# Kernel optimization log

Hardware: AMD Instinct MI355X
Metric: run time of the kernel (lower is better)

The kernel has to match this reference:

```python
import jax, jax.numpy as jnp
import numpy as np

EPS = 1e-6          # numerical floor for norms / denominators (fp32-safe)
PROJ_EPS = 1e-5     # ball projection margin: max norm = 1 - PROJ_EPS


def _norm(x):
    return jnp.sqrt(jnp.maximum(jnp.sum(x * x, axis=-1, keepdims=True), EPS * EPS))


def hyp_proj(x):
    # project onto open Poincare ball of radius 1 - PROJ_EPS
    n = _norm(x)
    scale = jnp.minimum((1.0 - PROJ_EPS) / n, 1.0)
    return x * scale


def exp_map_zero(v):
    n = _norm(v)
    return jnp.tanh(n) * v / n


def log_map_zero(y):
    n = _norm(y)
    return jnp.arctanh(jnp.minimum(n, 1.0 - PROJ_EPS)) * y / n


def mobius_add(x, y):
    x2 = jnp.sum(x * x, axis=-1, keepdims=True)
    y2 = jnp.sum(y * y, axis=-1, keepdims=True)
    xy = jnp.sum(x * y, axis=-1, keepdims=True)
    num = (1.0 + 2.0 * xy + y2) * x + (1.0 - x2) * y
    den = 1.0 + 2.0 * xy + x2 * y2
    return num / jnp.maximum(den, EPS)


def gcn_layer(x, rows, cols, vals, W, b, n_nodes, use_act):
    # tangent-space linear transform
    pre = log_map_zero(x)                      # [N, d]
    h = pre @ W                                # [N, d]
    # sparse adjacency matmul: agg[r] += val * h[c]
    msg = vals[:, None] * h[cols]              # [E, d]
    agg = jax.ops.segment_sum(msg, rows, num_segments=n_nodes)
    out = hyp_proj(exp_map_zero(agg))
    # hyperbolic bias via mobius addition
    bh = hyp_proj(exp_map_zero(b[None, :]))    # [1, d]
    out = hyp_proj(mobius_add(out, bh))
    if use_act:
        out = hyp_proj(exp_map_zero(jnp.tanh(log_map_zero(out))))
    return out


def setup_inputs() -> dict:
    key = jax.random.key(0)
    N, D, E = 100000, 64, 3200000
    ks = jax.random.split(key, 8)
    x = jax.random.normal(ks[0], (N, D), dtype=jnp.float32) * 0.1
    edge_vals = jax.random.uniform(ks[1], (E,), dtype=jnp.float32)
    W1 = jax.random.normal(ks[2], (D, D), dtype=jnp.float32) * (1.0 / np.sqrt(D))
    b1 = jnp.zeros((D,), dtype=jnp.float32)
    W2 = jax.random.normal(ks[3], (D, D), dtype=jnp.float32) * (1.0 / np.sqrt(D))
    b2 = jnp.zeros((D,), dtype=jnp.float32)
    edge_rows = jax.random.randint(ks[4], (E,), 0, N, dtype=jnp.int64 if jax.config.jax_enable_x64 else jnp.int32).astype(jnp.int32)
    edge_cols = jax.random.randint(ks[5], (E,), 0, N, dtype=jnp.int32)
    return {"x": x, "edge_vals": edge_vals, "W1": W1, "b1": b1,
            "W2": W2, "b2": b2, "edge_rows": edge_rows, "edge_cols": edge_cols}


def reference(x, edge_vals, W1, b1, W2, b2, edge_rows, edge_cols):
    n_nodes = x.shape[0]
    # HyperKA._graph_convolution: project base embeddings, then layers with
    # mobius residual; last layer has no activation.
    e0 = hyp_proj(x)
    h1 = gcn_layer(e0, edge_rows, edge_cols, edge_vals, W1, b1, n_nodes, use_act=True)
    h1 = hyp_proj(mobius_add(h1, e0))
    h2 = gcn_layer(h1, edge_rows, edge_cols, edge_vals, W2, b2, n_nodes, use_act=False)
    h2 = hyp_proj(mobius_add(h2, h1))
    return h2
```

## Files before the change

### kernel.cpp

```cpp
#include <hip/hip_runtime.h>
#include <math.h>

#define D 64
#define EPSF 1e-6f
#define EPS2F 1e-12f
#define PROJ_EPSF 1e-5f
#define EPB 16384

typedef _Float16 f16;
typedef f16 f16x4 __attribute__((ext_vector_type(4)));
typedef f16 f16x8 __attribute__((ext_vector_type(8)));
typedef float f32x4 __attribute__((ext_vector_type(4)));

__device__ __forceinline__ float frcp(float x)  { return __builtin_amdgcn_rcpf(x); }
__device__ __forceinline__ float fsqrt(float x) { return __builtin_amdgcn_sqrtf(x); }
__device__ __forceinline__ float ftanh(float x) {
    float e = __expf(2.0f * x);
    return (e - 1.0f) * frcp(e + 1.0f);
}
__device__ __forceinline__ float fatanh(float z) {
    return 0.5f * __logf((1.0f + z) * frcp(1.0f - z));
}

__device__ __forceinline__ float wave_sum(float v) {
#pragma unroll
    for (int o = 32; o > 0; o >>= 1) v += __shfl_xor(v, o, 64);
    return v;
}
__device__ __forceinline__ float qsum(float v) {
#pragma unroll
    for (int o = 1; o < 16; o <<= 1) v += __shfl_xor(v, o, 64);
    return v;
}

__global__ __launch_bounds__(256) void k1_hist_pre(
    const int* __restrict__ rows, const float* __restrict__ x,
    const float* __restrict__ b1, const float* __restrict__ b2,
    int* __restrict__ histT, f16* __restrict__ pre,
    float* __restrict__ nbuf, float* __restrict__ bhbuf,
    int E, int N, int nb1, int NBIN)
{
    const int bid = blockIdx.x, tid = threadIdx.x;
    const int lane = tid & 63;
    if (bid < nb1) {
        __shared__ int lh[512];
        for (int i = tid; i < NBIN; i += 256) lh[i] = 0;
        __syncthreads();
        const int e0 = bid * EPB;
#pragma unroll 4
        for (int k = 0; k < EPB / 256; ++k) {
            int e = e0 + k * 256 + tid;
            if (e < E) atomicAdd(&lh[__builtin_nontemporal_load(rows + e) >> 8], 1);
        }
        __syncthreads();
        for (int i = tid; i < NBIN; i += 256) histT[i * nb1 + bid] = lh[i];
    } else if (bid == nb1) {
        if (tid < 128) {
            int wsel = tid >> 6;
            const float* b = wsel ? b2 : b1;
            float bv = b[lane];
            float nb = fsqrt(fmaxf(wave_sum(bv * bv), EPS2F));
            float t = ftanh(nb);
            float v = bv * (t * frcp(nb));
            float nv = t;
            float sc = fminf((1.0f - PROJ_EPSF) * frcp(fmaxf(nv, EPSF)), 1.0f);
            v *= sc; nv = fminf(nv, 1.0f - PROJ_EPSF);
            bhbuf[wsel * 64 + lane] = v;
            if (lane == 0) bhbuf[128 + wsel] = nv;
        }
    } else {
        int node = (bid - nb1 - 1) * 4 + (tid >> 6);
        if (node >= N) return;
        float xv = x[(size_t)node * D + lane];
        float nx = fsqrt(fmaxf(wave_sum(xv * xv), EPS2F));
        float sc = fminf((1.0f - PROJ_EPSF) * frcp(nx), 1.0f);
        float e0 = xv * sc;
        float ne0 = fminf(nx, 1.0f - PROJ_EPSF);
        pre[(size_t)node * D + lane] = (f16)(e0 * (fatanh(ne0) * frcp(fmaxf(ne0, EPSF))));
        if (lane == 0) nbuf[node] = nx;
    }
}

__global__ __launch_bounds__(64) void scan_parts(int* __restrict__ part, int P)
{
    int lane = threadIdx.x;
    int carry = 0;
    for (int b = 0; b < P; b += 64) {
        int i = b + lane;
        int v = (i < P) ? part[i] : 0;
        int inc = v;
#pragma unroll
        for (int off = 1; off < 64; off <<= 1) {
            int tu = __shfl_up(inc, off, 64);
            if (lane >= off) inc += tu;
        }
        if (i < P) part[i] = inc - v + carry;
        carry += __shfl(inc, 63, 64);
    }
}

__global__ __launch_bounds__(256) void scan_apply(
    int* __restrict__ a, const int* __restrict__ part, int L)
{
    __shared__ int wbase[4];
    int t = threadIdx.x, lane = t & 63, wid = t >> 6;
    int idx0 = blockIdx.x * 1024 + t * 4;
    int v0 = 0, v1 = 0, v2 = 0, v3 = 0;
    if (idx0 < L) { int4 v = *(const int4*)(a + idx0); v0 = v.x; v1 = v.y; v2 = v.z; v3 = v.w; }
    int s = v0 + v1 + v2 + v3;
    int inc = s;
#pragma unroll
    for (int off = 1; off < 64; off <<= 1) {
        int tu = __shfl_up(inc, off, 64);
        if (lane >= off) inc += tu;
    }
    if (lane == 63) wbase[wid] = inc;
    __syncthreads();
    if (t == 0) { int acc = 0; for (int k = 0; k < 4; ++k) { int xx = wbase[k]; wbase[k] = acc; acc += xx; } }
    __syncthreads();
    int excl = part[blockIdx.x] + wbase[wid] + (inc - s);
    if (idx0 < L) {
        int4 o; o.x = excl; o.y = excl + v0; o.z = excl + v0 + v1; o.w = excl + v0 + v1 + v2;
        *(int4*)(a + idx0) = o;
    }
}

__device__ __forceinline__ void gemm64_body(
    const f16* __restrict__ A, const float* __restrict__ W,
    f16* __restrict__ C, int M, int wid, int nwaves, int lane)
{
    const int m = lane & 15;
    const int quad = lane >> 4;
    f16x8 Bfr[2][4];
#pragma unroll
    for (int kt = 0; kt < 2; ++kt)
#pragma unroll
        for (int nt = 0; nt < 4; ++nt) {
            f16x8 tmp;
#pragma unroll
            for (int j = 0; j < 8; ++j)
                tmp[j] = (f16)W[(kt * 32 + quad * 8 + j) * D + nt * 16 + m];
            Bfr[kt][nt] = tmp;
        }
    const int ntile = M >> 4;
    for (int tile = wid; tile < ntile; tile += nwaves) {
        const f16* arow = A + (size_t)(tile * 16 + m) * D;
        f16x8 a0 = *(const f16x8*)(arow + quad * 8);
        f16x8 a1 = *(const f16x8*)(arow + 32 + quad * 8);
#pragma unroll
        for (int nt = 0; nt < 4; ++nt) {
            f32x4 z = {0.0f, 0.0f, 0.0f, 0.0f};
            z = __builtin_amdgcn_mfma_f32_16x16x32_f16(a0, Bfr[0][nt], z, 0, 0, 0);
            z = __builtin_amdgcn_mfma_f32_16x16x32_f16(a1, Bfr[1][nt], z, 0, 0, 0);
#pragma unroll
            for (int r = 0; r < 4; ++r)
                C[(size_t)(tile * 16 + quad * 4 + r) * D + nt * 16 + m] = (f16)z[r];
        }
    }
}

__global__ __launch_bounds__(256) void k2_reduce_gemm(
    const int* __restrict__ histT, int* __restrict__ part, int Lp, int P,
    const f16* __restrict__ A, const float* __restrict__ W,
    f16* __restrict__ C, int M)
{
    const int tid = threadIdx.x, lane = tid & 63, wid4 = tid >> 6;
    if ((int)blockIdx.x < P) {
        __shared__ int ws[4];
        int idx0 = blockIdx.x * 1024 + tid * 4;
        int s = 0;
        if (idx0 < Lp) { int4 v = *(const int4*)(histT + idx0); s = v.x + v.y + v.z + v.w; }
        s = (int)wave_sum((float)s);
        if (lane == 0) ws[wid4] = s;
        __syncthreads();
        if (tid == 0) part[blockIdx.x] = ws[0] + ws[1] + ws[2] + ws[3];
    } else {
        int wid = (blockIdx.x - P) * 4 + wid4;
        int nwaves = (gridDim.x - P) * 4;
        gemm64_body(A, W, C, M, wid, nwaves, lane);
    }
}

__global__ __launch_bounds__(256) void gemm64(
    const f16* __restrict__ A, const float* __restrict__ W,
    f16* __restrict__ C, int M)
{
    gemm64_body(A, W, C, M, blockIdx.x * 4 + (threadIdx.x >> 6), gridDim.x * 4,
                threadIdx.x & 63);
}

__global__ __launch_bounds__(512) void p1_scatter(
    const int* __restrict__ rows, const int* __restrict__ cols,
    const float* __restrict__ vals, const int* __restrict__ histT,
    unsigned int* __restrict__ pay, unsigned char* __restrict__ rloc,
    int E, int nb1, int NBIN)
{
    __shared__ unsigned int  stage[512][32];
    __shared__ unsigned char srloc[512][32];
    __shared__ int gbase[512];
    __shared__ int cnt[512];
    __shared__ int flushed[512];
    __shared__ unsigned int msk[512];

    const int bid = blockIdx.x, tid = threadIdx.x;
    {
        int i = tid;
        gbase[i] = (i < NBIN) ? histT[i * nb1 + bid] : 0;
        cnt[i] = 0; flushed[i] = 0; msk[i] = 0u;
    }
    __syncthreads();

    const int e0 = bid * EPB;
    for (int rnd = 0; rnd < EPB / 2048; ++rnd) {
        int rr[4], cc[4]; float vv[4];
#pragma unroll
        for (int u = 0; u < 4; ++u) {
            int e = e0 + rnd * 2048 + u * 512 + tid;
            bool ok = e < E;
            rr[u] = ok ? __builtin_nontemporal_load(rows + e) : -1;
            cc[u] = ok ? __builtin_nontemporal_load(cols + e) : 0;
            vv[u] = ok ? __builtin_nontemporal_load(vals + e) : 0.0f;
        }
#pragma unroll
        for (int u = 0; u < 4; ++u) {
            if (rr[u] < 0) continue;
            int bin = rr[u] >> 8;
            unsigned int q = (unsigned int)fmaf(vv[u], 32767.0f, 0.5f);
            unsigned int p = (q << 17) | (unsigned int)cc[u];
            unsigned char rl = (unsigned char)(rr[u] & 255);
            int slot = atomicAdd(&cnt[bin], 1);
            if (slot - flushed[bin] < 32) {
                stage[bin][slot & 31] = p;
                srloc[bin][slot & 31] = rl;
                atomicOr(&msk[bin], 1u << (slot & 31));
            } else {
                int gp = gbase[bin] + slot;
                pay[gp] = p;
                rloc[gp] = rl;
            }
        }
        __syncthreads();
        if (tid < NBIN) {
            const int b = tid;
            int f = flushed[b];
            int n = cnt[b];
            unsigned int m = msk[b];
            const int gb = gbase[b];
            while (n - f >= 16) {
                const int half = (f >> 4) & 1;
                const unsigned int m16 = (m >> (half * 16)) & 0xFFFFu;
                const int base = gb + f;
                const int r0 = half * 16;
                if (m16 == 0xFFFFu) {
#pragma unroll
                    for (int k2 = 0; k2 < 16; ++k2)
                        pay[base + k2] = stage[b][r0 + k2];
#pragma unroll
                    for (int k2 = 0; k2 < 16; ++k2)
                        rloc[base + k2] = srloc[b][r0 + k2];
                } else {
                    for (int k2 = 0; k2 < 16; ++k2)
                        if (m16 & (1u << k2)) {
                            pay[base + k2] = stage[b][r0 + k2];
                            rloc[base + k2] = srloc[b][r0 + k2];
                        }
                }
                m &= ~(0xFFFFu << (half * 16));
                f += 16;
            }
            flushed[b] = f;
            msk[b] = m;
        }
        __syncthreads();
    }
    if (tid < NBIN) {
        const int b = tid;
        int f = flushed[b];
        const int n = cnt[b];
        const unsigned int m = msk[b];
        const int gb = gbase[b];
        for (; f < n; ++f) {
            if (m & (1u << (f & 31))) {
                pay[gb + f] = stage[b][f & 31];
                rloc[gb + f] = srloc[b][f & 31];
            }
        }
    }
}

__global__ __launch_bounds__(256) void band_build(
    const unsigned int* __restrict__ pay, const unsigned char* __restrict__ rloc,
    const int* __restrict__ histT, int* __restrict__ rs,
    unsigned int* __restrict__ epack, int E, int nb1, int NBIN, int N)
{
    __shared__ int lh[256];
    __shared__ int cur[256];
    __shared__ int wsum[4];
    const int b = blockIdx.x, tid = threadIdx.x;
    const int lane = tid & 63, wid = tid >> 6;
    const int segstart = histT[b * nb1];
    const int segend = (b + 1 < NBIN) ? histT[(b + 1) * nb1] : E;
    lh[tid] = 0;
    __syncthreads();
    for (int j = segstart + tid; j < segend; j += 256)
        atomicAdd(&lh[rloc[j]], 1);
    __syncthreads();
    int v = lh[tid];
    int inc = v;
#pragma unroll
    for (int off = 1; off < 64; off <<= 1) {
        int tu = __shfl_up(inc, off, 64);
        if (lane >= off) inc += tu;
    }
    if (lane == 63) wsum[wid] = inc;
    __syncthreads();
    int base = 0;
    for (int w2 = 0; w2 < wid; ++w2) base += wsum[w2];
    int excl = base + inc - v;
    cur[tid] = excl;
    int r = b * 256 + tid;
    if (r < N) rs[r] = segstart + excl + v;
    __syncthreads();
    for (int j = segstart + tid; j < segend; j += 256) {
        int pos = segstart + atomicAdd(&cur[rloc[j]], 1);
        epack[pos] = pay[j];
    }
}

__device__ __forceinline__ void csr_accum4(
    const int* __restrict__ rs, const unsigned int* __restrict__ epack,
    const f16* __restrict__ h, int row, int li, int qbase, float* a)
{
    const int start = (row == 0) ? 0 : rs[row - 1];
    const int end = rs[row];
    int nbat = (end - start + 15) >> 4;
#pragma unroll
    for (int o = 16; o < 64; o <<= 1) {
        int nbo = __shfl_xor(nbat, o, 64);
        nbat = nbo > nbat ? nbo : nbat;
    }
    const f16x4* __restrict__ h4 = (const f16x4*)h;
    float A0[4] = {0.f, 0.f, 0.f, 0.f}, A1[4] = {0.f, 0.f, 0.f, 0.f};
    for (int bb = 0; bb < nbat; ++bb) {
        int j = start + bb * 16 + li;
        unsigned int p = (j < end) ? epack[j] : 0u;
        int c = (int)(p & 131071u);
        float vf = (float)(p >> 17) * (1.0f / 32767.0f);
#pragma unroll
        for (int t = 0; t < 16; t += 2) {
            int   c0 = __shfl(c, qbase + t, 64);
            float v0 = __shfl(vf, qbase + t, 64);
            int   c1 = __shfl(c, qbase + t + 1, 64);
            float v1 = __shfl(vf, qbase + t + 1, 64);
            f16x4 h0 = h4[(size_t)c0 * 16 + li];
            f16x4 h1 = h4[(size_t)c1 * 16 + li];
#pragma unroll
            for (int k = 0; k < 4; ++k) {
                A0[k] = fmaf(v0, (float)h0[k], A0[k]);
                A1[k] = fmaf(v1, (float)h1[k], A1[k]);
            }
        }
    }
#pragma unroll
    for (int k = 0; k < 4; ++k) a[k] = A0[k] + A1[k];
}

__global__ __launch_bounds__(256) void layer1_fused(
    const int* __restrict__ rs, const unsigned int* __restrict__ epack,
    const f16* __restrict__ h, const float* __restrict__ x,
    const float* __restrict__ bhbuf, float* __restrict__ nbuf,
    f16* __restrict__ h1_out, f16* __restrict__ pre2_out, int N)
{
    const int lane = threadIdx.x & 63;
    const int q = lane >> 4, li = lane & 15, qbase = q << 4;
    int row = blockIdx.x * 16 + (threadIdx.x >> 6) * 4 + q;
    if (row >= N) row = N - 1;

    float a[4];
    csr_accum4(rs, epack, h, row, li, qbase, a);

    float na = fsqrt(fmaxf(qsum(a[0]*a[0] + a[1]*a[1] + a[2]*a[2] + a[3]*a[3]), EPS2F));
    float t = ftanh(na);
    float s = t * frcp(na);
    float o[4];
#pragma unroll
    for (int k = 0; k < 4; ++k) o[k] = a[k] * s;
    float no = t;
    float sc = fminf((1.0f - PROJ_EPSF) * frcp(fmaxf(no, EPSF)), 1.0f);
#pragma unroll
    for (int k = 0; k < 4; ++k) o[k] *= sc;
    no = fminf(no, 1.0f - PROJ_EPSF);

    float4 bp4 = ((const float4*)bhbuf)[li];
    float bh[4] = {bp4.x, bp4.y, bp4.z, bp4.w};
    float nbh = bhbuf[128];
    float xy = qsum(o[0]*bh[0] + o[1]*bh[1] + o[2]*bh[2] + o[3]*bh[3]);
    float x2 = no * no, y2 = nbh * nbh;
    float rd = frcp(fmaxf(1.0f + 2.0f * xy + x2 * y2, EPSF));
    float al = (1.0f + 2.0f * xy + y2) * rd;
    float be = (1.0f - x2) * rd;
    float m[4];
#pragma unroll
    for (int k = 0; k < 4; ++k) m[k] = al * o[k] + be * bh[k];
    float nm = fsqrt(fmaxf(al*al*x2 + be*be*y2 + 2.0f*al*be*xy, EPS2F));
    sc = fminf((1.0f - PROJ_EPSF) * frcp(fmaxf(nm, EPSF)), 1.0f);
#pragma unroll
    for (int k = 0; k < 4; ++k) m[k] *= sc;
    nm = fminf(nm, 1.0f - PROJ_EPSF);

    float lg = fatanh(nm) * frcp(fmaxf(nm, EPSF));
    float w[4];
#pragma unroll
    for (int k = 0; k < 4; ++k) w[k] = ftanh(m[k] * lg);
    float nw = fsqrt(fmaxf(qsum(w[0]*w[0] + w[1]*w[1] + w[2]*w[2] + w[3]*w[3]), EPS2F));
    float tw = ftanh(nw);
    s = tw * frcp(nw);
    float ov[4];
#pragma unroll
    for (int k = 0; k < 4; ++k) ov[k] = w[k] * s;
    float nov = tw;
    sc = fminf((1.0f - PROJ_EPSF) * frcp(fmaxf(nov, EPSF)), 1.0f);
#pragma unroll
    for (int k = 0; k < 4; ++k) ov[k] *= sc;
    nov = fminf(nov, 1.0f - PROJ_EPSF);

    float4 xp4 = ((const float4*)(x + (size_t)row * D))[li];
    float xp[4] = {xp4.x, xp4.y, xp4.z, xp4.w};
    float nx = nbuf[row];
    float sce = fminf((1.0f - PROJ_EPSF) * frcp(nx), 1.0f);
    float e0[4];
#pragma unroll
    for (int k = 0; k < 4; ++k) e0[k] = xp[k] * sce;
    float ne0 = fminf(nx, 1.0f - PROJ_EPSF);
    float xy2 = qsum(ov[0]*e0[0] + ov[1]*e0[1] + ov[2]*e0[2] + ov[3]*e0[3]);
    x2 = nov * nov; y2 = ne0 * ne0;
    rd = frcp(fmaxf(1.0f + 2.0f * xy2 + x2 * y2, EPSF));
    al = (1.0f + 2.0f * xy2 + y2) * rd;
    be = (1.0f - x2) * rd;
    float h1v[4];
#pragma unroll
    for (int k = 0; k < 4; ++k) h1v[k] = al * ov[k] + be * e0[k];
    float nh = fsqrt(fmaxf(al*al*x2 + be*be*y2 + 2.0f*al*be*xy2, EPS2F));
    sc = fminf((1.0f - PROJ_EPSF) * frcp(fmaxf(nh, EPSF)), 1.0f);
#pragma unroll
    for (int k = 0; k < 4; ++k) h1v[k] *= sc;
    nh = fminf(nh, 1.0f - PROJ_EPSF);

    f16x4 hp, pp;
    float lg2 = fatanh(nh) * frcp(fmaxf(nh, EPSF));
#pragma unroll
    for (int k = 0; k < 4; ++k) { hp[k] = (f16)h1v[k]; pp[k] = (f16)(h1v[k] * lg2); }
    ((f16x4*)h1_out)[(size_t)row * 16 + li] = hp;
    ((f16x4*)pre2_out)[(size_t)row * 16 + li] = pp;
    if (li == 0) nbuf[row] = nh;
}

__global__ __launch_bounds__(256) void layer2_fused(
    const int* __restrict__ rs, const unsigned int* __restrict__ epack,
    const f16* __restrict__ h2lin, const float* __restrict__ bhbuf,
    const float* __restrict__ nbuf, f16* __restrict__ h1_inout, int N)
{
    const int lane = threadIdx.x & 63;
    const int q = lane >> 4, li = lane & 15, qbase = q << 4;
    int row = blockIdx.x * 16 + (threadIdx.x >> 6) * 4 + q;
    if (row >= N) row = N - 1;

    float a[4];
    csr_accum4(rs, epack, h2lin, row, li, qbase, a);

    float na = fsqrt(fmaxf(qsum(a[0]*a[0] + a[1]*a[1] + a[2]*a[2] + a[3]*a[3]), EPS2F));
    float t = ftanh(na);
    float s = t * frcp(na);
    float o[4];
#pragma unroll
    for (int k = 0; k < 4; ++k) o[k] = a[k] * s;
    float no = t;
    float sc = fminf((1.0f - PROJ_EPSF) * frcp(fmaxf(no, EPSF)), 1.0f);
#pragma unroll
    for (int k = 0; k < 4; ++k) o[k] *= sc;
    no = fminf(no, 1.0f - PROJ_EPSF);

    float4 bp4 = ((const float4*)(bhbuf + 64))[li];
    float bh[4] = {bp4.x, bp4.y, bp4.z, bp4.w};
    float nbh = bhbuf[129];
    float xy = qsum(o[0]*bh[0] + o[1]*bh[1] + o[2]*bh[2] + o[3]*bh[3]);
    float x2 = no * no, y2 = nbh * nbh;
    float rd = frcp(fmaxf(1.0f + 2.0f * xy + x2 * y2, EPSF));
    float al = (1.0f + 2.0f * xy + y2) * rd;
    float be = (1.0f - x2) * rd;
    float m[4];
#pragma unroll
    for (int k = 0; k < 4; ++k) m[k] = al * o[k] + be * bh[k];
    float nm = fsqrt(fmaxf(al*al*x2 + be*be*y2 + 2.0f*al*be*xy, EPS2F));
    sc = fminf((1.0f - PROJ_EPSF) * frcp(fmaxf(nm, EPSF)), 1.0f);
#pragma unroll
    for (int k = 0; k < 4; ++k) m[k] *= sc;
    nm = fminf(nm, 1.0f - PROJ_EPSF);

    f16x4 hp = ((const f16x4*)h1_inout)[(size_t)row * 16 + li];
    float h1v[4] = {(float)hp[0], (float)hp[1], (float)hp[2], (float)hp[3]};
    float nh = nbuf[row];
    float xy2 = qsum(m[0]*h1v[0] + m[1]*h1v[1] + m[2]*h1v[2] + m[3]*h1v[3]);
    x2 = nm * nm; y2 = nh * nh;
    rd = frcp(fmaxf(1.0f + 2.0f * xy2 + x2 * y2, EPSF));
    al = (1.0f + 2.0f * xy2 + y2) * rd;
    be = (1.0f - x2) * rd;
    float r[4];
#pragma unroll
    for (int k = 0; k < 4; ++k) r[k] = al * m[k] + be * h1v[k];
    float n2 = fsqrt(fmaxf(al*al*x2 + be*be*y2 + 2.0f*al*be*xy2, EPS2F));
    sc = fminf((1.0f - PROJ_EPSF) * frcp(fmaxf(n2, EPSF)), 1.0f);
    f16x4 op;
#pragma unroll
    for (int k = 0; k < 4; ++k) op[k] = (f16)(r[k] * sc);
    ((f16x4*)h1_inout)[(size_t)row * 16 + li] = op;
}

__global__ __launch_bounds__(256) void expand4(
    const f16* __restrict__ src, float* __restrict__ dst, int n4)
{
    int i = blockIdx.x * 256 + threadIdx.x;
    if (i < n4) {
        f16x4 v = ((const f16x4*)src)[i];
        float4 o; o.x = (float)v[0]; o.y = (float)v[1]; o.z = (float)v[2]; o.w = (float)v[3];
        ((float4*)dst)[i] = o;
    }
}

extern "C" void kernel_launch(void* const* d_in, const int* in_sizes, int n_in,
                              void* d_out, int out_size, void* d_ws, size_t ws_size,
                              hipStream_t stream) {
    const float* x    = (const float*)d_in[0];
    const float* vals = (const float*)d_in[1];
    const float* W1   = (const float*)d_in[2];
    const float* b1   = (const float*)d_in[3];
    const float* W2   = (const float*)d_in[4];
    const float* b2   = (const float*)d_in[5];
    const int* rows   = (const int*)d_in[6];
    const int* cols   = (const int*)d_in[7];
    float* out = (float*)d_out;

    const int N = in_sizes[0] / D;
    const int E = in_sizes[1];
    const size_t nd = (size_t)N * D;

    const int NBIN = (N + 255) >> 8;
    const int nb1  = (E + EPB - 1) / EPB;
    const int L    = NBIN * nb1;
    const int Lp   = ((L + 1023) / 1024) * 1024;
    const int P    = Lp / 1024;

    char* w = (char*)d_ws;
    unsigned int*  epack = (unsigned int*)w;
    unsigned int*  pay   = (unsigned int*)(w + (size_t)E * 4);
    f16*           h1    = (f16*)(w + (size_t)E * 4);
    unsigned char* rloc  = (unsigned char*)(w + (size_t)E * 8);
    int*           histT = (int*)(w + (size_t)E * 9);
    size_t off = (size_t)E * 9 + (size_t)Lp * 4;
    int*   part  = (int*)(w + off);            off += 1024;
    int*   rs    = (int*)(w + off);            off += (size_t)N * 4;
    float* nbuf  = (float*)(w + off);          off += (size_t)N * 4;
    float* bhbuf = (float*)(w + off);

    f16* slot0 = (f16*)d_out;
    f16* slot1 = slot0 + nd;

    const int nbpre = (N + 3) / 4;
    const int nbq   = (N + 15) / 16;

    hipMemsetAsync(histT, 0, (size_t)Lp * 4, stream);
    k1_hist_pre<<<nb1 + 1 + nbpre, 256, 0, stream>>>(
        rows, x, b1, b2, histT, slot0, nbuf, bhbuf, E, N, nb1, NBIN);
    k2_reduce_gemm<<<P + 784, 256, 0, stream>>>(histT, part, Lp, P, slot0, W1, slot1, N);
    scan_parts<<<1, 64, 0, stream>>>(part, P);
    scan_apply<<<P, 256, 0, stream>>>(histT, part, Lp);
    p1_scatter<<<nb1, 512, 0, stream>>>(rows, cols, vals, histT, pay, rloc, E, nb1, NBIN);
    band_build<<<NBIN, 256, 0, stream>>>(pay, rloc, histT, rs, epack, E, nb1, NBIN, N);
    layer1_fused<<<nbq, 256, 0, stream>>>(rs, epack, slot1, x, bhbuf, nbuf, h1, slot0, N);
    gemm64<<<784, 256, 0, stream>>>(slot0, W2, slot1, N);
    layer2_fused<<<nbq, 256, 0, stream>>>(rs, epack, slot1, bhbuf, nbuf, h1, N);
    expand4<<<(int)((nd / 4 + 255) / 256), 256, 0, stream>>>(h1, out, (int)(nd / 4));
}
```

Baseline: 352.6 us.

## Fuse W2 GEMM into layer1, degree-sort rows, and broadcast edges via LDS

```diff
diff --git a/kernel.cpp b/kernel.cpp
--- a/kernel.cpp
+++ b/kernel.cpp
@@ -179,14 +179,6 @@
         int nwaves = (gridDim.x - P) * 4;
         gemm64_body(A, W, C, M, wid, nwaves, lane);
     }
-}
-
-__global__ __launch_bounds__(256) void gemm64(
-    const f16* __restrict__ A, const float* __restrict__ W,
-    f16* __restrict__ C, int M)
-{
-    gemm64_body(A, W, C, M, blockIdx.x * 4 + (threadIdx.x >> 6), gridDim.x * 4,
-                threadIdx.x & 63);
 }
 
 __global__ __launch_bounds__(512) void p1_scatter(
@@ -291,21 +283,26 @@
 __global__ __launch_bounds__(256) void band_build(
     const unsigned int* __restrict__ pay, const unsigned char* __restrict__ rloc,
     const int* __restrict__ histT, int* __restrict__ rs,
-    unsigned int* __restrict__ epack, int E, int nb1, int NBIN, int N)
+    unsigned int* __restrict__ epack, int* __restrict__ dhist,
+    int E, int nb1, int NBIN, int N)
 {
     __shared__ int lh[256];
     __shared__ int cur[256];
+    __shared__ int dh[256];
     __shared__ int wsum[4];
     const int b = blockIdx.x, tid = threadIdx.x;
     const int lane = tid & 63, wid = tid >> 6;
     const int segstart = histT[b * nb1];
     const int segend = (b + 1 < NBIN) ? histT[(b + 1) * nb1] : E;
     lh[tid] = 0;
+    dh[tid] = 0;
     __syncthreads();
     for (int j = segstart + tid; j < segend; j += 256)
         atomicAdd(&lh[rloc[j]], 1);
     __syncthreads();
     int v = lh[tid];
+    int r = b * 256 + tid;
+    if (r < N) atomicAdd(&dh[v > 255 ? 255 : v], 1);
     int inc = v;
 #pragma unroll
     for (int off = 1; off < 64; off <<= 1) {
@@ -318,18 +315,32 @@
     for (int w2 = 0; w2 < wid; ++w2) base += wsum[w2];
     int excl = base + inc - v;
     cur[tid] = excl;
-    int r = b * 256 + tid;
     if (r < N) rs[r] = segstart + excl + v;
     __syncthreads();
+    if (dh[tid] > 0) atomicAdd(&dhist[tid], dh[tid]);
     for (int j = segstart + tid; j < segend; j += 256) {
         int pos = segstart + atomicAdd(&cur[rloc[j]], 1);
         epack[pos] = pay[j];
     }
 }
 
+__global__ __launch_bounds__(256) void perm_scatter(
+    const int* __restrict__ rs, int* __restrict__ dhist,
+    int* __restrict__ perm, int N)
+{
+    int r = blockIdx.x * 256 + threadIdx.x;
+    if (r < N) {
+        int d = rs[r] - (r ? rs[r - 1] : 0);
+        if (d > 255) d = 255;
+        int pos = atomicAdd(&dhist[d], 1);
+        perm[pos] = r;
+    }
+}
+
 __device__ __forceinline__ void csr_accum4(
     const int* __restrict__ rs, const unsigned int* __restrict__ epack,
-    const f16* __restrict__ h, int row, int li, int qbase, float* a)
+    const f16* __restrict__ h, int row, int li, int2* __restrict__ qcv,
+    float* a)
 {
     const int start = (row == 0) ? 0 : rs[row - 1];
     const int end = rs[row];
@@ -344,16 +355,19 @@
     for (int bb = 0; bb < nbat; ++bb) {
         int j = start + bb * 16 + li;
         unsigned int p = (j < end) ? epack[j] : 0u;
-        int c = (int)(p & 131071u);
-        float vf = (float)(p >> 17) * (1.0f / 32767.0f);
+        int2 mycv;
+        mycv.x = (int)(p & 131071u);
+        mycv.y = __float_as_int((float)(p >> 17) * (1.0f / 32767.0f));
+        qcv[li] = mycv;
+        asm volatile("s_waitcnt lgkmcnt(0)" ::: "memory");
 #pragma unroll
         for (int t = 0; t < 16; t += 2) {
-            int   c0 = __shfl(c, qbase + t, 64);
-            float v0 = __shfl(vf, qbase + t, 64);
-            int   c1 = __shfl(c, qbase + t + 1, 64);
-            float v1 = __shfl(vf, qbase + t + 1, 64);
-            f16x4 h0 = h4[(size_t)c0 * 16 + li];
-            f16x4 h1 = h4[(size_t)c1 * 16 + li];
+            int2 cv0 = qcv[t];
+            int2 cv1 = qcv[t + 1];
+            f16x4 h0 = h4[(size_t)cv0.x * 16 + li];
+            f16x4 h1 = h4[(size_t)cv1.x * 16 + li];
+            float v0 = __int_as_float(cv0.y);
+            float v1 = __int_as_float(cv1.y);
 #pragma unroll
             for (int k = 0; k < 4; ++k) {
                 A0[k] = fmaf(v0, (float)h0[k], A0[k]);
@@ -369,15 +383,35 @@
     const int* __restrict__ rs, const unsigned int* __restrict__ epack,
     const f16* __restrict__ h, const float* __restrict__ x,
     const float* __restrict__ bhbuf, float* __restrict__ nbuf,
-    f16* __restrict__ h1_out, f16* __restrict__ pre2_out, int N)
-{
-    const int lane = threadIdx.x & 63;
-    const int q = lane >> 4, li = lane & 15, qbase = q << 4;
-    int row = blockIdx.x * 16 + (threadIdx.x >> 6) * 4 + q;
-    if (row >= N) row = N - 1;
+    const float* __restrict__ W2, const int* __restrict__ perm,
+    f16* __restrict__ h1_out, f16* __restrict__ h2lin, int N)
+{
+    __shared__ int2 cvs[16][16];
+    __shared__ f16 ptile[16 * 72];
+    __shared__ f16 w2l[D * D];
+    __shared__ int rowids[16];
+
+    const int tid = threadIdx.x;
+    const int lane = tid & 63;
+    const int q = lane >> 4, li = lane & 15;
+    const int rb = (tid >> 6) * 4 + q;
+    int prow = blockIdx.x * 16 + rb;
+    if (prow >= N) prow = N - 1;
+    const int row = perm[prow];
+
+    {
+        const float4* W4 = (const float4*)W2;
+        int i = tid;
+#pragma unroll
+        for (int it = 0; it < 4; ++it, i += 256) {
+            float4 v4 = W4[i];
+            f16x4 c4 = {(f16)v4.x, (f16)v4.y, (f16)v4.z, (f16)v4.w};
+            *(f16x4*)&w2l[i * 4] = c4;
+        }
+    }
 
     float a[4];
-    csr_accum4(rs, epack, h, row, li, qbase, a);
+    csr_accum4(rs, epack, h, row, li, &cvs[rb][0], a);
 
     float na = fsqrt(fmaxf(qsum(a[0]*a[0] + a[1]*a[1] + a[2]*a[2] + a[3]*a[3]), EPS2F));
     float t = ftanh(na);
@@ -451,22 +485,57 @@
 #pragma unroll
     for (int k = 0; k < 4; ++k) { hp[k] = (f16)h1v[k]; pp[k] = (f16)(h1v[k] * lg2); }
     ((f16x4*)h1_out)[(size_t)row * 16 + li] = hp;
-    ((f16x4*)pre2_out)[(size_t)row * 16 + li] = pp;
-    if (li == 0) nbuf[row] = nh;
+    *(f16x4*)&ptile[rb * 72 + li * 4] = pp;
+    if (li == 0) { rowids[rb] = row; nbuf[row] = nh; }
+    __syncthreads();
+
+    if (tid < 64) {
+        f16x8 B2[2][4];
+#pragma unroll
+        for (int kt = 0; kt < 2; ++kt)
+#pragma unroll
+            for (int nt = 0; nt < 4; ++nt) {
+                f16x8 tmp;
+#pragma unroll
+                for (int j = 0; j < 8; ++j)
+                    tmp[j] = w2l[(kt * 32 + q * 8 + j) * D + nt * 16 + li];
+                B2[kt][nt] = tmp;
+            }
+        f16x8 a0, a1;
+#pragma unroll
+        for (int j = 0; j < 8; ++j) {
+            a0[j] = ptile[li * 72 + q * 8 + j];
+            a1[j] = ptile[li * 72 + 32 + q * 8 + j];
+        }
+#pragma unroll
+        for (int nt = 0; nt < 4; ++nt) {
+            f32x4 z = {0.0f, 0.0f, 0.0f, 0.0f};
+            z = __builtin_amdgcn_mfma_f32_16x16x32_f16(a0, B2[0][nt], z, 0, 0, 0);
+            z = __builtin_amdgcn_mfma_f32_16x16x32_f16(a1, B2[1][nt], z, 0, 0, 0);
+#pragma unroll
+            for (int r = 0; r < 4; ++r)
+                h2lin[(size_t)rowids[q * 4 + r] * D + nt * 16 + li] = (f16)z[r];
+        }
+    }
 }
 
 __global__ __launch_bounds__(256) void layer2_fused(
     const int* __restrict__ rs, const unsigned int* __restrict__ epack,
     const f16* __restrict__ h2lin, const float* __restrict__ bhbuf,
-    const float* __restrict__ nbuf, f16* __restrict__ h1_inout, int N)
-{
-    const int lane = threadIdx.x & 63;
-    const int q = lane >> 4, li = lane & 15, qbase = q << 4;
-    int row = blockIdx.x * 16 + (threadIdx.x >> 6) * 4 + q;
-    if (row >= N) row = N - 1;
+    const float* __restrict__ nbuf, const int* __restrict__ perm,
+    f16* __restrict__ h1_inout, int N)
+{
+    __shared__ int2 cvs[16][16];
+    const int tid = threadIdx.x;
+    const int lane = tid & 63;
+    const int q = lane >> 4, li = lane & 15;
+    const int rb = (tid >> 6) * 4 + q;
+    int prow = blockIdx.x * 16 + rb;
+    if (prow >= N) prow = N - 1;
+    const int row = perm[prow];
 
     float a[4];
-    csr_accum4(rs, epack, h2lin, row, li, qbase, a);
+    csr_accum4(rs, epack, h2lin, row, li, &cvs[rb][0], a);
 
     float na = fsqrt(fmaxf(qsum(a[0]*a[0] + a[1]*a[1] + a[2]*a[2] + a[3]*a[3]), EPS2F));
     float t = ftanh(na);
@@ -556,11 +625,13 @@
     f16*           h1    = (f16*)(w + (size_t)E * 4);
     unsigned char* rloc  = (unsigned char*)(w + (size_t)E * 8);
     int*           histT = (int*)(w + (size_t)E * 9);
-    size_t off = (size_t)E * 9 + (size_t)Lp * 4;
+    int*           dhist = histT + Lp;
+    size_t off = (size_t)E * 9 + (size_t)Lp * 4 + 1024;
     int*   part  = (int*)(w + off);            off += 1024;
     int*   rs    = (int*)(w + off);            off += (size_t)N * 4;
     float* nbuf  = (float*)(w + off);          off += (size_t)N * 4;
-    float* bhbuf = (float*)(w + off);
+    float* bhbuf = (float*)(w + off);          off += 1024;
+    int*   perm  = (int*)(w + off);
 
     f16* slot0 = (f16*)d_out;
     f16* slot1 = slot0 + nd;
@@ -568,16 +639,18 @@
     const int nbpre = (N + 3) / 4;
     const int nbq   = (N + 15) / 16;
 
-    hipMemsetAsync(histT, 0, (size_t)Lp * 4, stream);
+    hipMemsetAsync(histT, 0, (size_t)Lp * 4 + 1024, stream);
     k1_hist_pre<<<nb1 + 1 + nbpre, 256, 0, stream>>>(
         rows, x, b1, b2, histT, slot0, nbuf, bhbuf, E, N, nb1, NBIN);
     k2_reduce_gemm<<<P + 784, 256, 0, stream>>>(histT, part, Lp, P, slot0, W1, slot1, N);
     scan_parts<<<1, 64, 0, stream>>>(part, P);
     scan_apply<<<P, 256, 0, stream>>>(histT, part, Lp);
     p1_scatter<<<nb1, 512, 0, stream>>>(rows, cols, vals, histT, pay, rloc, E, nb1, NBIN);
-    band_build<<<NBIN, 256, 0, stream>>>(pay, rloc, histT, rs, epack, E, nb1, NBIN, N);
-    layer1_fused<<<nbq, 256, 0, stream>>>(rs, epack, slot1, x, bhbuf, nbuf, h1, slot0, N);
-    gemm64<<<784, 256, 0, stream>>>(slot0, W2, slot1, N);
-    layer2_fused<<<nbq, 256, 0, stream>>>(rs, epack, slot1, bhbuf, nbuf, h1, N);
+    band_build<<<NBIN, 256, 0, stream>>>(pay, rloc, histT, rs, epack, dhist, E, nb1, NBIN, N);
+    scan_parts<<<1, 64, 0, stream>>>(dhist, 256);
+    perm_scatter<<<(N + 255) / 256, 256, 0, stream>>>(rs, dhist, perm, N);
+    layer1_fused<<<nbq, 256, 0, stream>>>(rs, epack, slot1, x, bhbuf, nbuf, W2, perm,
+                                          h1, slot0, N);
+    layer2_fused<<<nbq, 256, 0, stream>>>(rs, epack, slot0, bhbuf, nbuf, perm, h1, N);
     expand4<<<(int)((nd / 4 + 255) / 256), 256, 0, stream>>>(h1, out, (int)(nd / 4));
 }
```

After: 540.1 us. 53.2% more time.
